# Optimization experiments

Hardware: AMD Instinct MI355X
Metric: run time of the kernel (lower is better)

## Reference

```python
import jax, jax.numpy as jnp
import numpy as np

B, T, N = 16, 12, 1024
DIM_IN, DOUT, CHEB_K, EMB = 1, 64, 2, 10
TOD, DOW = 48, 7
DIN = DIM_IN + 2 * EMB  # 21: input feature + tod emb + dow emb


def _mk(key, shape, scale=0.1):
    return scale * jax.random.normal(key, shape, dtype=jnp.float32)


def setup_inputs() -> dict:
    key = jax.random.key(0)
    ks = jax.random.split(key, 16)
    data = jax.random.normal(ks[0], (B, T, N, DIM_IN), jnp.float32)
    tod = jax.random.randint(ks[1], (B, T, N), 0, TOD).astype(jnp.float32)
    dow = jax.random.randint(ks[2], (B, T, N), 0, DOW).astype(jnp.float32)
    x = jnp.concatenate([data, tod[..., None], dow[..., None]], axis=-1)
    return dict(
        x=x,
        init_state=jnp.zeros((1, B, N, DOUT), jnp.float32),
        ne_tod=jax.random.normal(ks[3], (B, T, EMB), jnp.float32),
        ne_dow=jax.random.normal(ks[4], (B, T, EMB), jnp.float32),
        node_emb=jax.random.normal(ks[5], (N, EMB), jnp.float32),
        Wtod=_mk(ks[6], (TOD, EMB)), btod=jnp.zeros((EMB,), jnp.float32),
        Wdow=_mk(ks[7], (DOW, EMB)), bdow=jnp.zeros((EMB,), jnp.float32),
        WQ=_mk(ks[8], (DOUT, DOUT)), bQ=jnp.zeros((DOUT,), jnp.float32),
        WK=_mk(ks[9], (DOUT, DOUT)), bK=jnp.zeros((DOUT,), jnp.float32),
        WV=_mk(ks[10], (DOUT, DOUT)), bV=jnp.zeros((DOUT,), jnp.float32),
        Wpool_g=_mk(ks[11], (EMB, CHEB_K, DIN + DOUT, 2 * DOUT)),
        bpool_g=_mk(ks[12], (EMB, 2 * DOUT)),
        Wpool_c=_mk(ks[13], (EMB, CHEB_K, DIN + DOUT, DOUT)),
        bpool_c=_mk(ks[14], (EMB, DOUT)),
    )


def _cheb(A, x):
    # Chebyshev basis: T0=x, T1=A@x, Tk=2A T_{k-1}-T_{k-2}. A:[B,N,N], x:[B,N,F] -> [B,K,N,F]
    outs = [x, jnp.einsum('bnm,bmf->bnf', A, x)]
    for _ in range(CHEB_K - 2):
        outs.append(2.0 * jnp.einsum('bnm,bmf->bnf', A, outs[-1]) - outs[-2])
    return jnp.stack(outs[:CHEB_K], axis=1)


def _gconv(A, x, W, b):
    # node-adaptive graph conv: W:[N,K,F,O] (per-node weights from pool), b:[N,O]
    return jnp.einsum('bknf,nkfo->bno', _cheb(A, x), W) + b


def reference(x, init_state, ne_tod, ne_dow, node_emb, Wtod, btod, Wdow, bdow,
              WQ, bQ, WK, bK, WV, bV, Wpool_g, bpool_g, Wpool_c, bpool_c):
    tod = x[..., -2].astype(jnp.int32)
    dow = x[..., -1].astype(jnp.int32)
    # one_hot @ Linear == embedding gather (same math)
    cur = jnp.concatenate([x[..., :DIM_IN], Wtod[tod] + btod, Wdow[dow] + bdow], axis=-1)

    E = node_emb
    # per-node weights/bias from pools (static over time -> hoisted out of scan)
    Wg = jnp.einsum('nd,dkfo->nkfo', E, Wpool_g)
    bg = E @ bpool_g
    Wc = jnp.einsum('nd,dkfo->nkfo', E, Wpool_c)
    bc = E @ bpool_c

    def step(h, inputs):
        x_t, e1, e2 = inputs
        # dynamic adjacency from time-modulated node embeddings
        d1 = E[None] * e1[:, None, :]  # B,N,d
        d2 = E[None] * e2[:, None, :]
        A = jax.nn.softmax(jax.nn.relu(jnp.einsum('bnd,bmd->bnm', d1, d2)), axis=-1)
        zr = jax.nn.sigmoid(_gconv(A, jnp.concatenate([x_t, h], -1), Wg, bg))
        z, r = jnp.split(zr, 2, axis=-1)
        hc = jnp.tanh(_gconv(A, jnp.concatenate([x_t, z * h], -1), Wc, bc))
        h_new = r * h + (1.0 - r) * hc
        return h_new, h_new

    xs = (jnp.moveaxis(cur, 1, 0), jnp.moveaxis(ne_tod, 1, 0), jnp.moveaxis(ne_dow, 1, 0))
    h_last, states = jax.lax.scan(step, init_state[0], xs)
    seq = jnp.moveaxis(states, 0, 1)  # B,T,N,DOUT

    # temporal self-attention (per node, over T)
    xr = jnp.swapaxes(seq, 1, 2)  # B,N,T,DOUT
    Q = xr @ WQ + bQ
    K = xr @ WK + bK
    V = xr @ WV + bV
    attn = jax.nn.softmax(jnp.einsum('bntd,bnsd->bnts', Q, K) / (DOUT ** 0.5), axis=-1)
    Z = jnp.einsum('bnts,bnsd->bntd', attn, V)
    out = jnp.swapaxes(Z, 1, 2)  # B,T,N,DOUT
    return out, h_last
```

## Files before the change

kernel.cpp:

```cpp
#include <hip/hip_runtime.h>

#define BB 16
#define TT 12
#define NN 1024
#define EMB 10
#define DIN 21
#define DOUT 64
#define FF 85
#define FP 96
#define KFP 176
#define BTN (BB * TT * NN)
#define ASCALE 256.0f
#define INV_ASCALE (1.0f / 256.0f)
#define LSCALE 4096.0f
#define INV_LSCALE (1.0f / 4096.0f)

typedef float4 f4;
typedef _Float16 f16;
typedef __attribute__((ext_vector_type(8))) _Float16 f16x8;
typedef __attribute__((ext_vector_type(4))) float f32x4;

__global__ __launch_bounds__(256) void k_embedT(const float* __restrict__ x,
    const float* __restrict__ Wtod, const float* __restrict__ btod,
    const float* __restrict__ Wdow, const float* __restrict__ bdow,
    f16* __restrict__ curh, f16* __restrict__ curl) {
  int idx = blockIdx.x * 256 + threadIdx.x;
  if (idx >= BB * TT * DIN * NN) return;
  int n = idx & 1023;
  int f = (idx >> 10) % DIN;
  int bt = idx / (DIN * 1024);
  const float* xp = x + ((size_t)bt * 1024 + n) * 3;
  float v;
  if (f == 0) v = xp[0];
  else if (f < 1 + EMB) {
    int tod = (int)xp[1];
    v = Wtod[tod * EMB + f - 1] + btod[f - 1];
  } else {
    int dow = (int)xp[2];
    v = Wdow[dow * EMB + f - 1 - EMB] + bdow[f - 1 - EMB];
  }
  f16 hi = (f16)v;
  curh[idx] = hi;
  curl[idx] = (f16)((v - (float)hi) * LSCALE);
}

__global__ __launch_bounds__(256) void k_wpT(const float* __restrict__ Wpool,
    float* __restrict__ Wp2, int O, int total) {
  int idx = blockIdx.x * 256 + threadIdx.x;
  if (idx >= total) return;
  int j = idx & 7;
  int d = (idx >> 3) % EMB;
  int kc = (idx / (8 * EMB)) % 22;
  int o = idx / (8 * EMB * 22);
  int kf = kc * 8 + j;
  Wp2[idx] = (kf < 2 * FF) ? Wpool[((size_t)d * 2 * FF + kf) * O + o] : 0.f;
}

__global__ __launch_bounds__(256) void k_poolT(const float* __restrict__ E,
    const float* __restrict__ Wp2, f16* __restrict__ Wh, f16* __restrict__ Wl,
    int O, int CH) {
  int n0 = blockIdx.y * 16;
  int c = blockIdx.x * 256 + threadIdx.x;
  __shared__ float Es[16][EMB];
  if (threadIdx.x < 16 * EMB)
    Es[threadIdx.x / EMB][threadIdx.x % EMB] =
        E[(n0 + threadIdx.x / EMB) * EMB + threadIdx.x % EMB];
  __syncthreads();
  if (c >= CH) return;
  const float* wb = Wp2 + (size_t)c * 80;
  float wv[80];
#pragma unroll
  for (int i = 0; i < 20; i++) *(f4*)&wv[i * 4] = *(const f4*)(wb + i * 4);
  for (int ni = 0; ni < 16; ni++) {
    f16x8 hv, lv;
#pragma unroll
    for (int j = 0; j < 8; j++) {
      float v = 0.f;
#pragma unroll
      for (int d = 0; d < EMB; d++) v = fmaf(Es[ni][d], wv[d * 8 + j], v);
      f16 hi = (f16)v;
      hv[j] = hi;
      lv[j] = (f16)((v - (float)hi) * LSCALE);
    }
    size_t base = ((size_t)(n0 + ni) * O * 22 + c) * 8;
    *(f16x8*)(Wh + base) = hv;
    *(f16x8*)(Wl + base) = lv;
  }
}

__global__ __launch_bounds__(256) void k_poolb(const float* __restrict__ E,
    const float* __restrict__ bpool, float* __restrict__ bvec, int O) {
  int idx = blockIdx.x * 256 + threadIdx.x;
  if (idx >= NN * O) return;
  int o = idx % O, n = idx / O;
  float a = 0.f;
#pragma unroll
  for (int d = 0; d < EMB; d++) a += E[n * EMB + d] * bpool[d * O + o];
  bvec[idx] = a;
}

__global__ __launch_bounds__(256) void k_inith(const float* __restrict__ s,
    float* __restrict__ hb, f16* __restrict__ hTh, f16* __restrict__ hTl) {
  int i = blockIdx.x * 256 + threadIdx.x;
  if (i >= BB * NN * DOUT) return;
  float v = s[i];
  hb[i] = v;
  int b = i >> 16;
  int n = (i >> 6) & 1023;
  int o = i & 63;
  f16 hi = (f16)v;
  size_t ti = (((size_t)(b * 64 + o)) << 10) + n;
  hTh[ti] = hi;
  hTl[ti] = (f16)((v - (float)hi) * LSCALE);
}

__global__ __launch_bounds__(256) void k_cvtw(const float* __restrict__ WQ,
    const float* __restrict__ WK, const float* __restrict__ WV,
    const float* __restrict__ bQ, const float* __restrict__ bK, const float* __restrict__ bV,
    f16* __restrict__ wbt, float* __restrict__ biasb) {
  int idx = blockIdx.x * 256 + threadIdx.x;
  if (idx < 3 * DOUT * DOUT) {
    int mat = idx >> 12;
    int d = (idx >> 6) & 63;
    int k = idx & 63;
    const float* W = mat == 0 ? WQ : (mat == 1 ? WK : WV);
    wbt[idx] = (f16)(W[k * DOUT + d]);
  } else if (idx < 3 * DOUT * DOUT + 192) {
    int j = idx - 3 * DOUT * DOUT;
    const float* bb = (j >> 6) == 0 ? bQ : ((j >> 6) == 1 ? bK : bV);
    biasb[j] = bb[j & 63];
  }
}

__global__ __launch_bounds__(256) void k_scores(const float* __restrict__ E,
    const float* __restrict__ ne1, const float* __restrict__ ne2, int t,
    f16* __restrict__ Ah,
    float* __restrict__ T1g, float* __restrict__ T1c) {
  int b = blockIdx.y;
  int i0 = blockIdx.x * 4;
  int tid = threadIdx.x;
  int lane = tid & 63;
  int wid = tid >> 6;
  {
    int gid = (blockIdx.y * gridDim.x + blockIdx.x) * 256 + tid;
    for (int i = gid; i < BB * NN * FP; i += 1048576) T1g[i] = 0.f;
    T1c[gid] = 0.f;
  }
  __shared__ float redm[4][4];
  __shared__ float reds[4][4];
  float g[EMB];
#pragma unroll
  for (int d = 0; d < EMB; d++)
    g[d] = ne1[(b * TT + t) * EMB + d] * ne2[(b * TT + t) * EMB + d];
  float c[4][EMB];
#pragma unroll
  for (int ii = 0; ii < 4; ii++)
#pragma unroll
    for (int d = 0; d < EMB; d++)
      c[ii][d] = E[(i0 + ii) * EMB + d] * g[d];
  float s[4][4];
#pragma unroll
  for (int jj = 0; jj < 4; jj++) {
    int j = jj * 256 + tid;
    float Ej[EMB];
#pragma unroll
    for (int d = 0; d < EMB; d++) Ej[d] = E[j * EMB + d];
#pragma unroll
    for (int ii = 0; ii < 4; ii++) {
      float acc = 0.f;
#pragma unroll
      for (int d = 0; d < EMB; d++) acc = fmaf(c[ii][d], Ej[d], acc);
      s[ii][jj] = fmaxf(acc, 0.f);
    }
  }
  float m4[4];
#pragma unroll
  for (int ii = 0; ii < 4; ii++) {
    float v = fmaxf(fmaxf(s[ii][0], s[ii][1]), fmaxf(s[ii][2], s[ii][3]));
#pragma unroll
    for (int off = 32; off > 0; off >>= 1) v = fmaxf(v, __shfl_xor(v, off));
    if (lane == 0) redm[wid][ii] = v;
  }
  __syncthreads();
#pragma unroll
  for (int ii = 0; ii < 4; ii++)
    m4[ii] = fmaxf(fmaxf(redm[0][ii], redm[1][ii]), fmaxf(redm[2][ii], redm[3][ii]));
  float e[4][4];
  float inv[4];
#pragma unroll
  for (int ii = 0; ii < 4; ii++) {
    float lsum = 0.f;
#pragma unroll
    for (int jj = 0; jj < 4; jj++) { e[ii][jj] = __expf(s[ii][jj] - m4[ii]); lsum += e[ii][jj]; }
#pragma unroll
    for (int off = 32; off > 0; off >>= 1) lsum += __shfl_xor(lsum, off);
    if (lane == 0) reds[wid][ii] = lsum;
  }
  __syncthreads();
#pragma unroll
  for (int ii = 0; ii < 4; ii++)
    inv[ii] = ASCALE / (reds[0][ii] + reds[1][ii] + reds[2][ii] + reds[3][ii]);
#pragma unroll
  for (int ii = 0; ii < 4; ii++) {
    size_t base = ((size_t)(b * NN) + i0 + ii) * NN;
#pragma unroll
    for (int jj = 0; jj < 4; jj++) {
      Ah[base + jj * 256 + tid] = (f16)(e[ii][jj] * inv[ii]);
    }
  }
}

__global__ __launch_bounds__(256) void k_spmv_g(
    const f16* __restrict__ Ah,
    const f16* __restrict__ curh, const f16* __restrict__ curl, int t,
    const f16* __restrict__ hTh, const f16* __restrict__ hTl,
    float* __restrict__ Y) {
  int b = blockIdx.y;
  int i0 = blockIdx.x * 32;
  int kh = blockIdx.z;
  int tid = threadIdx.x;
  int lane = tid & 63, w = tid >> 6;
  int rg = w & 1, cg = w >> 1;
  int quad = lane >> 4, m = lane & 15;
  __shared__ __align__(16) f16 As_h[32][72];
  __shared__ __align__(16) f16 Xh[96][72];
  __shared__ __align__(16) f16 Xl[96][72];
  for (int q = tid; q < 11 * 72; q += 256) {
    int f = 85 + q / 72, j = q % 72;
    Xh[f][j] = (f16)0.f;
    Xl[f][j] = (f16)0.f;
  }
  f32x4 accH[3], accL[3];
#pragma unroll
  for (int q = 0; q < 3; q++) {
    accH[q] = (f32x4){0.f, 0.f, 0.f, 0.f};
    accL[q] = (f32x4){0.f, 0.f, 0.f, 0.f};
  }
  const f16* Ahb = Ah + ((size_t)(b * NN + i0)) * NN;
  const f16* curhb = curh + ((size_t)(b * TT + t) * DIN) * NN;
  const f16* curlb = curl + ((size_t)(b * TT + t) * DIN) * NN;
  const f16* hThb = hTh + ((size_t)b << 16);
  const f16* hTlb = hTl + ((size_t)b << 16);
  int ar = tid >> 3, ac = (tid & 7) << 3;
  for (int j0 = kh * 512; j0 < kh * 512 + 512; j0 += 64) {
    *(int4*)&As_h[ar][ac] = *(const int4*)(Ahb + (size_t)ar * NN + j0 + ac);
#pragma unroll
    for (int p = 0; p < 6; p++) {
      int ch = p * 256 + tid;
      int isl = ch >= 768 ? 1 : 0;
      int idx = ch - isl * 768;
      int row = idx >> 3, cc = (idx & 7) << 3;
      if (row < 85) {
        const f16* s = row < 21
            ? ((isl ? curlb : curhb) + ((size_t)row << 10) + j0 + cc)
            : ((isl ? hTlb : hThb) + ((size_t)(row - 21) << 10) + j0 + cc);
        f16* d = (isl ? &Xl[0][0] : &Xh[0][0]) + row * 72 + cc;
        *(int4*)d = *(const int4*)s;
      }
    }
    __syncthreads();
#pragma unroll
    for (int ks = 0; ks < 2; ks++) {
      int k0 = ks * 32 + quad * 8;
      f16x8 a_h = *(const f16x8*)&As_h[rg * 16 + m][k0];
#pragma unroll
      for (int nfi = 0; nfi < 3; nfi++) {
        int nf = cg * 3 + nfi;
        f16x8 x_h = *(const f16x8*)&Xh[nf * 16 + m][k0];
        f16x8 x_l = *(const f16x8*)&Xl[nf * 16 + m][k0];
        accH[nfi] = __builtin_amdgcn_mfma_f32_16x16x32_f16(a_h, x_h, accH[nfi], 0, 0, 0);
        accL[nfi] = __builtin_amdgcn_mfma_f32_16x16x32_f16(a_h, x_l, accL[nfi], 0, 0, 0);
      }
    }
    __syncthreads();
  }
#pragma unroll
  for (int nfi = 0; nfi < 3; nfi++) {
    int nf = cg * 3 + nfi;
#pragma unroll
    for (int reg = 0; reg < 4; reg++) {
      int row = i0 + rg * 16 + quad * 4 + reg;
      atomicAdd(&Y[((size_t)(b * NN) + row) * FP + nf * 16 + m],
                (accH[nfi][reg] + accL[nfi][reg] * INV_LSCALE) * INV_ASCALE);
    }
  }
}

__global__ __launch_bounds__(256) void k_spmv_c(
    const f16* __restrict__ Ah,
    const f16* __restrict__ zhTh, const f16* __restrict__ zhTl,
    float* __restrict__ Y) {
  int b = blockIdx.y;
  int i0 = blockIdx.x * 32;
  int kh = blockIdx.z;
  int tid = threadIdx.x;
  int lane = tid & 63, w = tid >> 6;
  int rg = w & 1, cg = w >> 1;
  int quad = lane >> 4, m = lane & 15;
  __shared__ __align__(16) f16 As_h[32][72];
  __shared__ __align__(16) f16 Xh[64][72];
  __shared__ __align__(16) f16 Xl[64][72];
  f32x4 accH[2], accL[2];
#pragma unroll
  for (int q = 0; q < 2; q++) {
    accH[q] = (f32x4){0.f, 0.f, 0.f, 0.f};
    accL[q] = (f32x4){0.f, 0.f, 0.f, 0.f};
  }
  const f16* Ahb = Ah + ((size_t)(b * NN + i0)) * NN;
  const f16* zThb = zhTh + ((size_t)b << 16);
  const f16* zTlb = zhTl + ((size_t)b << 16);
  int ar = tid >> 3, ac = (tid & 7) << 3;
  for (int j0 = kh * 512; j0 < kh * 512 + 512; j0 += 64) {
    *(int4*)&As_h[ar][ac] = *(const int4*)(Ahb + (size_t)ar * NN + j0 + ac);
#pragma unroll
    for (int p = 0; p < 4; p++) {
      int ch = p * 256 + tid;
      int isl = ch >= 512 ? 1 : 0;
      int idx = ch - isl * 512;
      int row = idx >> 3, cc = (idx & 7) << 3;
      const f16* s = (isl ? zTlb : zThb) + ((size_t)row << 10) + j0 + cc;
      f16* d = (isl ? &Xl[0][0] : &Xh[0][0]) + row * 72 + cc;
      *(int4*)d = *(const int4*)s;
    }
    __syncthreads();
#pragma unroll
    for (int ks = 0; ks < 2; ks++) {
      int k0 = ks * 32 + quad * 8;
      f16x8 a_h = *(const f16x8*)&As_h[rg * 16 + m][k0];
#pragma unroll
      for (int nfi = 0; nfi < 2; nfi++) {
        int nf = cg * 2 + nfi;
        f16x8 x_h = *(const f16x8*)&Xh[nf * 16 + m][k0];
        f16x8 x_l = *(const f16x8*)&Xl[nf * 16 + m][k0];
        accH[nfi] = __builtin_amdgcn_mfma_f32_16x16x32_f16(a_h, x_h, accH[nfi], 0, 0, 0);
        accL[nfi] = __builtin_amdgcn_mfma_f32_16x16x32_f16(a_h, x_l, accL[nfi], 0, 0, 0);
      }
    }
    __syncthreads();
  }
#pragma unroll
  for (int nfi = 0; nfi < 2; nfi++) {
    int nf = cg * 2 + nfi;
#pragma unroll
    for (int reg = 0; reg < 4; reg++) {
      int row = i0 + rg * 16 + quad * 4 + reg;
      atomicAdd(&Y[(((size_t)(b * NN) + row) << 6) + nf * 16 + m],
                (accH[nfi][reg] + accL[nfi][reg] * INV_LSCALE) * INV_ASCALE);
    }
  }
}

__global__ __launch_bounds__(256) void k_nodemm_g(
    const f16* __restrict__ curh, const f16* __restrict__ curl, int t,
    const float* __restrict__ hb, const float* __restrict__ T1,
    const f16* __restrict__ Wh, const f16* __restrict__ Wl,
    const float* __restrict__ bg,
    float* __restrict__ r, float* __restrict__ zhb,
    f16* __restrict__ zhTh, f16* __restrict__ zhTl) {
  int n = (blockIdx.x & 7) * 128 + (blockIdx.x >> 3);
  int oc = blockIdx.y;
  int tid = threadIdx.x;
  int lane = tid & 63, w = tid >> 6;
  int quad = lane >> 4, m = lane & 15;
  __shared__ __align__(16) f16 Xh[16][200];
  __shared__ __align__(16) f16 Xl[16][200];
  for (int q = tid; q < 16 * 200; q += 256) {
    int bi = q / 200, kf = q % 200;
    f16 hi, lo;
    if (kf < DIN) {
      size_t ci = (((size_t)(bi * TT + t) * DIN) + kf) * NN + n;
      hi = curh[ci];
      lo = curl[ci];
    } else if (kf < 2 * FF) {
      float v = (kf < FF) ? hb[(((size_t)bi << 10) + n) * DOUT + kf - DIN]
                          : T1[(((size_t)bi << 10) + n) * FP + kf - FF];
      hi = (f16)v;
      lo = (f16)((v - (float)hi) * LSCALE);
    } else {
      hi = (f16)0.f;
      lo = (f16)0.f;
    }
    Xh[bi][kf] = hi;
    Xl[bi][kf] = lo;
  }
  __syncthreads();
  f32x4 accH = (f32x4){0.f, 0.f, 0.f, 0.f};
  f32x4 accL = (f32x4){0.f, 0.f, 0.f, 0.f};
  const f16* WhB = Wh + ((size_t)(n * 128 + oc * 64 + w * 16 + m)) * KFP + quad * 8;
  const f16* WlB = Wl + ((size_t)(n * 128 + oc * 64 + w * 16 + m)) * KFP + quad * 8;
#pragma unroll
  for (int ks = 0; ks < 6; ks++) {
    f16x8 b_h = *(const f16x8*)(WhB + ks * 32);
    f16x8 b_l = *(const f16x8*)(WlB + ks * 32);
    int k0 = ks * 32 + quad * 8;
    f16x8 a_h = *(const f16x8*)&Xh[m][k0];
    f16x8 a_l = *(const f16x8*)&Xl[m][k0];
    accH = __builtin_amdgcn_mfma_f32_16x16x32_f16(a_h, b_h, accH, 0, 0, 0);
    accL = __builtin_amdgcn_mfma_f32_16x16x32_f16(a_h, b_l, accL, 0, 0, 0);
    accL = __builtin_amdgcn_mfma_f32_16x16x32_f16(a_l, b_h, accL, 0, 0, 0);
  }
  int o = oc * 64 + w * 16 + m;
  float bias = bg[n * 128 + o];
  if (oc == 0) {
#pragma unroll
    for (int reg = 0; reg < 4; reg++) {
      int bi = quad * 4 + reg;
      float v = accH[reg] + accL[reg] * INV_LSCALE + bias;
      v = 1.f / (1.f + __expf(-v));
      size_t off = (((size_t)bi << 10) + n) * DOUT;
      float zh = v * hb[off + o];
      zhb[off + o] = zh;
      f16 hi = (f16)zh;
      size_t ti = (((size_t)(bi * 64 + o)) << 10) + n;
      zhTh[ti] = hi;
      zhTl[ti] = (f16)((zh - (float)hi) * LSCALE);
    }
  } else {
#pragma unroll
    for (int reg = 0; reg < 4; reg++) {
      int bi = quad * 4 + reg;
      float v = accH[reg] + accL[reg] * INV_LSCALE + bias;
      v = 1.f / (1.f + __expf(-v));
      r[(((size_t)bi << 10) + n) * DOUT + o - DOUT] = v;
    }
  }
}

__global__ __launch_bounds__(256) void k_nodemm_c(
    const f16* __restrict__ curh, const f16* __restrict__ curl, int t,
    const float* __restrict__ hb_in, const float* __restrict__ zhb,
    const float* __restrict__ T1g, const float* __restrict__ T1c,
    const f16* __restrict__ Wh, const f16* __restrict__ Wl,
    const float* __restrict__ bc,
    const float* __restrict__ r, float* __restrict__ hb, f16* __restrict__ seqb,
    f16* __restrict__ hTh, f16* __restrict__ hTl) {
  int n = (blockIdx.x & 7) * 128 + (blockIdx.x >> 3);
  int tid = threadIdx.x;
  int lane = tid & 63, w = tid >> 6;
  int quad = lane >> 4, m = lane & 15;
  __shared__ __align__(16) f16 Xh[16][200];
  __shared__ __align__(16) f16 Xl[16][200];
  for (int q = tid; q < 16 * 200; q += 256) {
    int bi = q / 200, kf = q % 200;
    f16 hi, lo;
    if (kf < DIN) {
      size_t ci = (((size_t)(bi * TT + t) * DIN) + kf) * NN + n;
      hi = curh[ci];
      lo = curl[ci];
    } else if (kf < 2 * FF) {
      float v;
      if (kf < FF) v = zhb[(((size_t)bi << 10) + n) * DOUT + kf - DIN];
      else {
        int u = kf - FF;
        v = (u < DIN) ? T1g[(((size_t)bi << 10) + n) * FP + u]
                      : T1c[((((size_t)bi << 10) + n) << 6) + (u - DIN)];
      }
      hi = (f16)v;
      lo = (f16)((v - (float)hi) * LSCALE);
    } else {
      hi = (f16)0.f;
      lo = (f16)0.f;
    }
    Xh[bi][kf] = hi;
    Xl[bi][kf] = lo;
  }
  __syncthreads();
  f32x4 accH = (f32x4){0.f, 0.f, 0.f, 0.f};
  f32x4 accL = (f32x4){0.f, 0.f, 0.f, 0.f};
  const f16* WhB = Wh + ((size_t)(n * 64 + w * 16 + m)) * KFP + quad * 8;
  const f16* WlB = Wl + ((size_t)(n * 64 + w * 16 + m)) * KFP + quad * 8;
#pragma unroll
  for (int ks = 0; ks < 6; ks++) {
    f16x8 b_h = *(const f16x8*)(WhB + ks * 32);
    f16x8 b_l = *(const f16x8*)(WlB + ks * 32);
    int k0 = ks * 32 + quad * 8;
    f16x8 a_h = *(const f16x8*)&Xh[m][k0];
    f16x8 a_l = *(const f16x8*)&Xl[m][k0];
    accH = __builtin_amdgcn_mfma_f32_16x16x32_f16(a_h, b_h, accH, 0, 0, 0);
    accL = __builtin_amdgcn_mfma_f32_16x16x32_f16(a_h, b_l, accL, 0, 0, 0);
    accL = __builtin_amdgcn_mfma_f32_16x16x32_f16(a_l, b_h, accL, 0, 0, 0);
  }
  int o = w * 16 + m;
  float bias = bc[n * 64 + o];
#pragma unroll
  for (int reg = 0; reg < 4; reg++) {
    int bi = quad * 4 + reg;
    float v = accH[reg] + accL[reg] * INV_LSCALE + bias;
    float hc = tanhf(v);
    size_t off = (((size_t)bi << 10) + n) * DOUT + o;
    float rv = r[off];
    float hn = rv * hb_in[off] + (1.f - rv) * hc;
    hb[off] = hn;
    seqb[((size_t)(bi * TT + t) * NN + n) * DOUT + o] = (f16)hn;
    f16 hi = (f16)hn;
    size_t ti = (((size_t)(bi * 64 + o)) << 10) + n;
    hTh[ti] = hi;
    hTl[ti] = (f16)((hn - (float)hi) * LSCALE);
  }
}

__global__ __launch_bounds__(256) void k_qkv(const f16* __restrict__ seqb,
    const f16* __restrict__ wbt, const float* __restrict__ biasb,
    f16* __restrict__ qkvb) {
  int R0 = blockIdx.x * 128;
  int tid = threadIdx.x;
  int lane = tid & 63, w = tid >> 6;
  int quad = lane >> 4, m = lane & 15;
  __shared__ __align__(16) f16 Sb[128][72];
  __shared__ __align__(16) f16 Wt[192][72];
#pragma unroll
  for (int p = 0; p < 4; p++) {
    int q = p * 256 + tid;
    int rr = q >> 3, cc = q & 7;
    *(int4*)&Sb[rr][cc * 8] = *(const int4*)&seqb[((size_t)(R0 + rr) << 6) + cc * 8];
  }
#pragma unroll
  for (int p = 0; p < 6; p++) {
    int q = p * 256 + tid;
    int rr = q >> 3, cc = q & 7;
    *(int4*)&Wt[rr][cc * 8] = *(const int4*)&wbt[((size_t)rr << 6) + cc * 8];
  }
  __syncthreads();
  f32x4 acc[2][12];
#pragma unroll
  for (int mi = 0; mi < 2; mi++)
#pragma unroll
    for (int nf = 0; nf < 12; nf++) acc[mi][nf] = (f32x4){0.f, 0.f, 0.f, 0.f};
#pragma unroll
  for (int ks = 0; ks < 2; ks++) {
    int k0 = ks * 32 + quad * 8;
    f16x8 a0 = *(const f16x8*)&Sb[w * 32 + m][k0];
    f16x8 a1 = *(const f16x8*)&Sb[w * 32 + 16 + m][k0];
#pragma unroll
    for (int nf = 0; nf < 12; nf++) {
      f16x8 bb = *(const f16x8*)&Wt[nf * 16 + m][k0];
      acc[0][nf] = __builtin_amdgcn_mfma_f32_16x16x32_f16(a0, bb, acc[0][nf], 0, 0, 0);
      acc[1][nf] = __builtin_amdgcn_mfma_f32_16x16x32_f16(a1, bb, acc[1][nf], 0, 0, 0);
    }
  }
  float bias_r[12];
#pragma unroll
  for (int nf = 0; nf < 12; nf++) bias_r[nf] = biasb[nf * 16 + m];
#pragma unroll
  for (int mi = 0; mi < 2; mi++) {
#pragma unroll
    for (int nf = 0; nf < 12; nf++) {
      int mat = nf >> 2;
      int d = (nf & 3) * 16 + m;
#pragma unroll
      for (int reg = 0; reg < 4; reg++) {
        int R = R0 + w * 32 + mi * 16 + quad * 4 + reg;
        qkvb[(size_t)mat * BTN * DOUT + ((size_t)R << 6) + d] = (f16)(acc[mi][nf][reg] + bias_r[nf]);
      }
    }
  }
}

__global__ __launch_bounds__(256) void k_attn2(const f16* __restrict__ qkvb,
    float* __restrict__ out) {
  int wv = threadIdx.x >> 6;
  int d = threadIdx.x & 63;
  int n = blockIdx.x * 4 + wv;
  int b = blockIdx.y;
  const f16* Qb = qkvb;
  const f16* Kb = qkvb + (size_t)BTN * DOUT;
  const f16* Vb = qkvb + (size_t)2 * BTN * DOUT;
  __shared__ f16 Qs[4][TT][72], Ks[4][TT][72];
  __shared__ float at[4][TT][13];
  float vr[TT];
#pragma unroll
  for (int t = 0; t < TT; t++) {
    size_t off = ((size_t)(b * TT + t) * NN + n) * DOUT + d;
    Qs[wv][t][d] = Qb[off];
    Ks[wv][t][d] = Kb[off];
    vr[t] = (float)Vb[off];
  }
  __syncthreads();
  for (int idx = d; idx < TT * TT; idx += 64) {
    int tt = idx / TT, ss = idx % TT;
    float sc = 0.f;
#pragma unroll
    for (int k = 0; k < DOUT; k++)
      sc = fmaf((float)Qs[wv][tt][k], (float)Ks[wv][ss][k], sc);
    at[wv][tt][ss] = sc * 0.125f;
  }
  __syncthreads();
  if (d < TT) {
    float mx = -1e30f;
#pragma unroll
    for (int s = 0; s < TT; s++) mx = fmaxf(mx, at[wv][d][s]);
    float sum = 0.f;
#pragma unroll
    for (int s = 0; s < TT; s++) { float e = __expf(at[wv][d][s] - mx); at[wv][d][s] = e; sum += e; }
    float inv = 1.f / sum;
#pragma unroll
    for (int s = 0; s < TT; s++) at[wv][d][s] *= inv;
  }
  __syncthreads();
  float o[TT];
#pragma unroll
  for (int t = 0; t < TT; t++) o[t] = 0.f;
#pragma unroll
  for (int s = 0; s < TT; s++) {
    float vv = vr[s];
#pragma unroll
    for (int t = 0; t < TT; t++) o[t] = fmaf(at[wv][t][s], vv, o[t]);
  }
#pragma unroll
  for (int t = 0; t < TT; t++)
    out[((size_t)(b * TT + t) * NN + n) * DOUT + d] = o[t];
}

__global__ __launch_bounds__(256) void k_hlast(const float* __restrict__ h, float* __restrict__ o) {
  int i = blockIdx.x * 256 + threadIdx.x;
  if (i < BB * NN * DOUT) o[i] = h[i];
}

extern "C" void kernel_launch(void* const* d_in, const int* in_sizes, int n_in,
                              void* d_out, int out_size, void* d_ws, size_t ws_size,
                              hipStream_t stream) {
  const float* x        = (const float*)d_in[0];
  const float* init_st  = (const float*)d_in[1];
  const float* ne_tod   = (const float*)d_in[2];
  const float* ne_dow   = (const float*)d_in[3];
  const float* E        = (const float*)d_in[4];
  const float* Wtod     = (const float*)d_in[5];
  const float* btod     = (const float*)d_in[6];
  const float* Wdow     = (const float*)d_in[7];
  const float* bdow     = (const float*)d_in[8];
  const float* WQ       = (const float*)d_in[9];
  const float* bQ       = (const float*)d_in[10];
  const float* WK       = (const float*)d_in[11];
  const float* bK       = (const float*)d_in[12];
  const float* WV       = (const float*)d_in[13];
  const float* bV       = (const float*)d_in[14];
  const float* Wpool_g  = (const float*)d_in[15];
  const float* bpool_g  = (const float*)d_in[16];
  const float* Wpool_c  = (const float*)d_in[17];
  const float* bpool_c  = (const float*)d_in[18];

  float* out = (float*)d_out;
  float* hlast_out = out + (size_t)BTN * DOUT;
  f16* seqb = (f16*)d_out;

  char* P = (char*)d_ws;
  auto alloc = [&](size_t bytes) { char* r = P; P += (bytes + 255) & ~(size_t)255; return r; };
  f16* curh  = (f16*)alloc((size_t)BB * TT * DIN * NN * 2);
  f16* curl  = (f16*)alloc((size_t)BB * TT * DIN * NN * 2);
  f16* Wgh   = (f16*)alloc((size_t)NN * 128 * KFP * 2);
  f16* Wgl   = (f16*)alloc((size_t)NN * 128 * KFP * 2);
  f16* Wch   = (f16*)alloc((size_t)NN * 64 * KFP * 2);
  f16* Wcl   = (f16*)alloc((size_t)NN * 64 * KFP * 2);
  float* Wp2g = (float*)alloc((size_t)128 * 22 * EMB * 8 * 4);
  float* Wp2c = (float*)alloc((size_t)64 * 22 * EMB * 8 * 4);
  float* bg  = (float*)alloc((size_t)NN * 128 * 4);
  float* bc  = (float*)alloc((size_t)NN * 64 * 4);
  float* hb  = (float*)alloc((size_t)BB * NN * DOUT * 4);
  f16* wbt   = (f16*)alloc((size_t)3 * DOUT * DOUT * 2);
  float* biasb = (float*)alloc(192 * 4);
  float* rb  = (float*)alloc((size_t)BB * NN * DOUT * 4);
  float* zhb = (float*)alloc((size_t)BB * NN * DOUT * 4);
  f16* hTh   = (f16*)alloc((size_t)BB * DOUT * NN * 2);
  f16* hTl   = (f16*)alloc((size_t)BB * DOUT * NN * 2);
  f16* zhTh  = (f16*)alloc((size_t)BB * DOUT * NN * 2);
  f16* zhTl  = (f16*)alloc((size_t)BB * DOUT * NN * 2);
  char* LOOP = P;
  f16* Ah    = (f16*)alloc((size_t)BB * NN * NN * 2);
  float* T1g = (float*)alloc((size_t)BB * NN * FP * 4);
  float* T1c = (float*)alloc((size_t)BB * NN * DOUT * 4);
  f16* qkvb  = (f16*)LOOP;

  k_embedT<<<(BB * TT * DIN * NN + 255) / 256, 256, 0, stream>>>(x, Wtod, btod, Wdow, bdow, curh, curl);
  {
    int totg = 128 * 22 * EMB * 8;
    int totc = 64 * 22 * EMB * 8;
    k_wpT<<<(totg + 255) / 256, 256, 0, stream>>>(Wpool_g, Wp2g, 128, totg);
    k_wpT<<<(totc + 255) / 256, 256, 0, stream>>>(Wpool_c, Wp2c, 64, totc);
  }
  k_poolT<<<dim3(11, 64), 256, 0, stream>>>(E, Wp2g, Wgh, Wgl, 128, 128 * 22);
  k_poolT<<<dim3(6, 64), 256, 0, stream>>>(E, Wp2c, Wch, Wcl, 64, 64 * 22);
  k_poolb<<<(NN * 128 + 255) / 256, 256, 0, stream>>>(E, bpool_g, bg, 128);
  k_poolb<<<(NN * 64 + 255) / 256, 256, 0, stream>>>(E, bpool_c, bc, 64);
  k_inith<<<(BB * NN * DOUT + 255) / 256, 256, 0, stream>>>(init_st, hb, hTh, hTl);
  k_cvtw<<<(3 * DOUT * DOUT + 192 + 255) / 256, 256, 0, stream>>>(WQ, WK, WV, bQ, bK, bV, wbt, biasb);

  for (int t = 0; t < TT; t++) {
    k_scores<<<dim3(NN / 4, BB), 256, 0, stream>>>(E, ne_tod, ne_dow, t, Ah, T1g, T1c);
    k_spmv_g<<<dim3(NN / 32, BB, 2), 256, 0, stream>>>(Ah, curh, curl, t, hTh, hTl, T1g);
    k_nodemm_g<<<dim3(NN, 2), 256, 0, stream>>>(curh, curl, t, hb, T1g, Wgh, Wgl, bg, rb, zhb, zhTh, zhTl);
    k_spmv_c<<<dim3(NN / 32, BB, 2), 256, 0, stream>>>(Ah, zhTh, zhTl, T1c);
    k_nodemm_c<<<NN, 256, 0, stream>>>(curh, curl, t, hb, zhb, T1g, T1c, Wch, Wcl, bc, rb, hb, seqb, hTh, hTl);
  }

  k_qkv<<<BTN / 128, 256, 0, stream>>>(seqb, wbt, biasb, qkvb);
  k_attn2<<<dim3(NN / 4, BB), 256, 0, stream>>>(qkvb, out);
  k_hlast<<<(BB * NN * DOUT + 255) / 256, 256, 0, stream>>>(hb, hlast_out);
}
```

Baseline: 1.748 ms.

## Fuse next-step adjacency scores and T1 zeroing into candidate node-GEMM kernel

The separate per-step k_scores launch is replaced. The next timestep's softmax adjacency is now computed by extra blocks appended to the candidate-state node-GEMM kernel, and each node block zeroes its own T1g/T1c rows after staging them into shared memory. A single k_scores call before the loop handles step 0. This removes one kernel launch per timestep and lets score computation overlap with the GEMM work, in exchange for a larger, heterogeneous grid and relying on Ah not being read during the current step's final kernel.

```diff
diff --git a/kernel.cpp b/kernel.cpp
--- a/kernel.cpp
+++ b/kernel.cpp
@@ -135,13 +135,13 @@
 __global__ __launch_bounds__(256) void k_scores(const float* __restrict__ E,
     const float* __restrict__ ne1, const float* __restrict__ ne2, int t,
     f16* __restrict__ Ah,
-    float* __restrict__ T1g, float* __restrict__ T1c) {
+    float* __restrict__ T1g, float* __restrict__ T1c, int zfill) {
   int b = blockIdx.y;
   int i0 = blockIdx.x * 4;
   int tid = threadIdx.x;
   int lane = tid & 63;
   int wid = tid >> 6;
-  {
+  if (zfill) {
     int gid = (blockIdx.y * gridDim.x + blockIdx.x) * 256 + tid;
     for (int i = gid; i < BB * NN * FP; i += 1048576) T1g[i] = 0.f;
     T1c[gid] = 0.f;
@@ -426,76 +426,158 @@
   }
 }
 
-__global__ __launch_bounds__(256) void k_nodemm_c(
+__global__ __launch_bounds__(256) void k_ncsc(
     const f16* __restrict__ curh, const f16* __restrict__ curl, int t,
     const float* __restrict__ hb_in, const float* __restrict__ zhb,
-    const float* __restrict__ T1g, const float* __restrict__ T1c,
+    float* __restrict__ T1g, float* __restrict__ T1c,
     const f16* __restrict__ Wh, const f16* __restrict__ Wl,
     const float* __restrict__ bc,
     const float* __restrict__ r, float* __restrict__ hb, f16* __restrict__ seqb,
-    f16* __restrict__ hTh, f16* __restrict__ hTl) {
-  int n = (blockIdx.x & 7) * 128 + (blockIdx.x >> 3);
+    f16* __restrict__ hTh, f16* __restrict__ hTl,
+    const float* __restrict__ E, const float* __restrict__ ne1,
+    const float* __restrict__ ne2, f16* __restrict__ Ah) {
   int tid = threadIdx.x;
-  int lane = tid & 63, w = tid >> 6;
-  int quad = lane >> 4, m = lane & 15;
   __shared__ __align__(16) f16 Xh[16][200];
   __shared__ __align__(16) f16 Xl[16][200];
-  for (int q = tid; q < 16 * 200; q += 256) {
-    int bi = q / 200, kf = q % 200;
-    f16 hi, lo;
-    if (kf < DIN) {
-      size_t ci = (((size_t)(bi * TT + t) * DIN) + kf) * NN + n;
-      hi = curh[ci];
-      lo = curl[ci];
-    } else if (kf < 2 * FF) {
-      float v;
-      if (kf < FF) v = zhb[(((size_t)bi << 10) + n) * DOUT + kf - DIN];
-      else {
-        int u = kf - FF;
-        v = (u < DIN) ? T1g[(((size_t)bi << 10) + n) * FP + u]
-                      : T1c[((((size_t)bi << 10) + n) << 6) + (u - DIN)];
+  __shared__ float redm[4][4];
+  __shared__ float reds[4][4];
+  if (blockIdx.x < NN) {
+    int n = (blockIdx.x & 7) * 128 + (blockIdx.x >> 3);
+    int lane = tid & 63, w = tid >> 6;
+    int quad = lane >> 4, m = lane & 15;
+    for (int q = tid; q < 16 * 200; q += 256) {
+      int bi = q / 200, kf = q % 200;
+      f16 hi, lo;
+      if (kf < DIN) {
+        size_t ci = (((size_t)(bi * TT + t) * DIN) + kf) * NN + n;
+        hi = curh[ci];
+        lo = curl[ci];
+      } else if (kf < 2 * FF) {
+        float v;
+        if (kf < FF) v = zhb[(((size_t)bi << 10) + n) * DOUT + kf - DIN];
+        else {
+          int u = kf - FF;
+          v = (u < DIN) ? T1g[(((size_t)bi << 10) + n) * FP + u]
+                        : T1c[((((size_t)bi << 10) + n) << 6) + (u - DIN)];
+        }
+        hi = (f16)v;
+        lo = (f16)((v - (float)hi) * LSCALE);
+      } else {
+        hi = (f16)0.f;
+        lo = (f16)0.f;
       }
-      hi = (f16)v;
-      lo = (f16)((v - (float)hi) * LSCALE);
-    } else {
-      hi = (f16)0.f;
-      lo = (f16)0.f;
-    }
-    Xh[bi][kf] = hi;
-    Xl[bi][kf] = lo;
-  }
-  __syncthreads();
-  f32x4 accH = (f32x4){0.f, 0.f, 0.f, 0.f};
-  f32x4 accL = (f32x4){0.f, 0.f, 0.f, 0.f};
-  const f16* WhB = Wh + ((size_t)(n * 64 + w * 16 + m)) * KFP + quad * 8;
-  const f16* WlB = Wl + ((size_t)(n * 64 + w * 16 + m)) * KFP + quad * 8;
-#pragma unroll
-  for (int ks = 0; ks < 6; ks++) {
-    f16x8 b_h = *(const f16x8*)(WhB + ks * 32);
-    f16x8 b_l = *(const f16x8*)(WlB + ks * 32);
-    int k0 = ks * 32 + quad * 8;
-    f16x8 a_h = *(const f16x8*)&Xh[m][k0];
-    f16x8 a_l = *(const f16x8*)&Xl[m][k0];
-    accH = __builtin_amdgcn_mfma_f32_16x16x32_f16(a_h, b_h, accH, 0, 0, 0);
-    accL = __builtin_amdgcn_mfma_f32_16x16x32_f16(a_h, b_l, accL, 0, 0, 0);
-    accL = __builtin_amdgcn_mfma_f32_16x16x32_f16(a_l, b_h, accL, 0, 0, 0);
-  }
-  int o = w * 16 + m;
-  float bias = bc[n * 64 + o];
-#pragma unroll
-  for (int reg = 0; reg < 4; reg++) {
-    int bi = quad * 4 + reg;
-    float v = accH[reg] + accL[reg] * INV_LSCALE + bias;
-    float hc = tanhf(v);
-    size_t off = (((size_t)bi << 10) + n) * DOUT + o;
-    float rv = r[off];
-    float hn = rv * hb_in[off] + (1.f - rv) * hc;
-    hb[off] = hn;
-    seqb[((size_t)(bi * TT + t) * NN + n) * DOUT + o] = (f16)hn;
-    f16 hi = (f16)hn;
-    size_t ti = (((size_t)(bi * 64 + o)) << 10) + n;
-    hTh[ti] = hi;
-    hTl[ti] = (f16)((hn - (float)hi) * LSCALE);
+      Xh[bi][kf] = hi;
+      Xl[bi][kf] = lo;
+    }
+    __syncthreads();
+    for (int q = tid; q < BB * FP; q += 256) {
+      int bi = q / FP, col = q % FP;
+      T1g[(((size_t)bi << 10) + n) * FP + col] = 0.f;
+    }
+    for (int q = tid; q < BB * DOUT; q += 256) {
+      int bi = q >> 6, col = q & 63;
+      T1c[((((size_t)bi << 10) + n) << 6) + col] = 0.f;
+    }
+    f32x4 accH = (f32x4){0.f, 0.f, 0.f, 0.f};
+    f32x4 accL = (f32x4){0.f, 0.f, 0.f, 0.f};
+    const f16* WhB = Wh + ((size_t)(n * 64 + w * 16 + m)) * KFP + quad * 8;
+    const f16* WlB = Wl + ((size_t)(n * 64 + w * 16 + m)) * KFP + quad * 8;
+#pragma unroll
+    for (int ks = 0; ks < 6; ks++) {
+      f16x8 b_h = *(const f16x8*)(WhB + ks * 32);
+      f16x8 b_l = *(const f16x8*)(WlB + ks * 32);
+      int k0 = ks * 32 + quad * 8;
+      f16x8 a_h = *(const f16x8*)&Xh[m][k0];
+      f16x8 a_l = *(const f16x8*)&Xl[m][k0];
+      accH = __builtin_amdgcn_mfma_f32_16x16x32_f16(a_h, b_h, accH, 0, 0, 0);
+      accL = __builtin_amdgcn_mfma_f32_16x16x32_f16(a_h, b_l, accL, 0, 0, 0);
+      accL = __builtin_amdgcn_mfma_f32_16x16x32_f16(a_l, b_h, accL, 0, 0, 0);
+    }
+    int o = w * 16 + m;
+    float bias = bc[n * 64 + o];
+#pragma unroll
+    for (int reg = 0; reg < 4; reg++) {
+      int bi = quad * 4 + reg;
+      float v = accH[reg] + accL[reg] * INV_LSCALE + bias;
+      float hc = tanhf(v);
+      size_t off = (((size_t)bi << 10) + n) * DOUT + o;
+      float rv = r[off];
+      float hn = rv * hb_in[off] + (1.f - rv) * hc;
+      hb[off] = hn;
+      seqb[((size_t)(bi * TT + t) * NN + n) * DOUT + o] = (f16)hn;
+      f16 hi = (f16)hn;
+      size_t ti = (((size_t)(bi * 64 + o)) << 10) + n;
+      hTh[ti] = hi;
+      hTl[ti] = (f16)((hn - (float)hi) * LSCALE);
+    }
+  } else {
+    int ts = t + 1;
+    if (ts >= TT) return;
+    int sidx = blockIdx.x - NN;
+    int b = sidx >> 8;
+    int i0 = (sidx & 255) * 4;
+    int lane = tid & 63;
+    int wid = tid >> 6;
+    float g[EMB];
+#pragma unroll
+    for (int d = 0; d < EMB; d++)
+      g[d] = ne1[(b * TT + ts) * EMB + d] * ne2[(b * TT + ts) * EMB + d];
+    float c[4][EMB];
+#pragma unroll
+    for (int ii = 0; ii < 4; ii++)
+#pragma unroll
+      for (int d = 0; d < EMB; d++)
+        c[ii][d] = E[(i0 + ii) * EMB + d] * g[d];
+    float s[4][4];
+#pragma unroll
+    for (int jj = 0; jj < 4; jj++) {
+      int j = jj * 256 + tid;
+      float Ej[EMB];
+#pragma unroll
+      for (int d = 0; d < EMB; d++) Ej[d] = E[j * EMB + d];
+#pragma unroll
+      for (int ii = 0; ii < 4; ii++) {
+        float acc = 0.f;
+#pragma unroll
+        for (int d = 0; d < EMB; d++) acc = fmaf(c[ii][d], Ej[d], acc);
+        s[ii][jj] = fmaxf(acc, 0.f);
+      }
+    }
+    float m4[4];
+#pragma unroll
+    for (int ii = 0; ii < 4; ii++) {
+      float v = fmaxf(fmaxf(s[ii][0], s[ii][1]), fmaxf(s[ii][2], s[ii][3]));
+#pragma unroll
+      for (int off = 32; off > 0; off >>= 1) v = fmaxf(v, __shfl_xor(v, off));
+      if (lane == 0) redm[wid][ii] = v;
+    }
+    __syncthreads();
+#pragma unroll
+    for (int ii = 0; ii < 4; ii++)
+      m4[ii] = fmaxf(fmaxf(redm[0][ii], redm[1][ii]), fmaxf(redm[2][ii], redm[3][ii]));
+    float e[4][4];
+    float inv[4];
+#pragma unroll
+    for (int ii = 0; ii < 4; ii++) {
+      float lsum = 0.f;
+#pragma unroll
+      for (int jj = 0; jj < 4; jj++) { e[ii][jj] = __expf(s[ii][jj] - m4[ii]); lsum += e[ii][jj]; }
+#pragma unroll
+      for (int off = 32; off > 0; off >>= 1) lsum += __shfl_xor(lsum, off);
+      if (lane == 0) reds[wid][ii] = lsum;
+    }
+    __syncthreads();
+#pragma unroll
+    for (int ii = 0; ii < 4; ii++)
+      inv[ii] = ASCALE / (reds[0][ii] + reds[1][ii] + reds[2][ii] + reds[3][ii]);
+#pragma unroll
+    for (int ii = 0; ii < 4; ii++) {
+      size_t base = ((size_t)(b * NN) + i0 + ii) * NN;
+#pragma unroll
+      for (int jj = 0; jj < 4; jj++) {
+        Ah[base + jj * 256 + tid] = (f16)(e[ii][jj] * inv[ii]);
+      }
+    }
   }
 }
 
@@ -684,12 +766,13 @@
   k_inith<<<(BB * NN * DOUT + 255) / 256, 256, 0, stream>>>(init_st, hb, hTh, hTl);
   k_cvtw<<<(3 * DOUT * DOUT + 192 + 255) / 256, 256, 0, stream>>>(WQ, WK, WV, bQ, bK, bV, wbt, biasb);
 
+  k_scores<<<dim3(NN / 4, BB), 256, 0, stream>>>(E, ne_tod, ne_dow, 0, Ah, T1g, T1c, 1);
   for (int t = 0; t < TT; t++) {
-    k_scores<<<dim3(NN / 4, BB), 256, 0, stream>>>(E, ne_tod, ne_dow, t, Ah, T1g, T1c);
     k_spmv_g<<<dim3(NN / 32, BB, 2), 256, 0, stream>>>(Ah, curh, curl, t, hTh, hTl, T1g);
     k_nodemm_g<<<dim3(NN, 2), 256, 0, stream>>>(curh, curl, t, hb, T1g, Wgh, Wgl, bg, rb, zhb, zhTh, zhTl);
     k_spmv_c<<<dim3(NN / 32, BB, 2), 256, 0, stream>>>(Ah, zhTh, zhTl, T1c);
-    k_nodemm_c<<<NN, 256, 0, stream>>>(curh, curl, t, hb, zhb, T1g, T1c, Wch, Wcl, bc, rb, hb, seqb, hTh, hTl);
+    k_ncsc<<<NN + (NN / 4) * BB, 256, 0, stream>>>(curh, curl, t, hb, zhb, T1g, T1c,
+        Wch, Wcl, bc, rb, hb, seqb, hTh, hTl, E, ne_tod, ne_dow, Ah);
   }
 
   k_qkv<<<BTN / 128, 256, 0, stream>>>(seqb, wbt, biasb, qkvb);
```

New measurement: 1.687 ms. 1.04x faster.
